# Kernel tuning notes

Hardware: AMD Instinct MI355X
Metric: run time of the kernel (lower is better)

Reference implementation:

```python
import jax, jax.numpy as jnp
import numpy as np

B, T, V, H = 4, 512, 8000, 7


def setup_inputs() -> dict:
    key = jax.random.key(0)
    k1, k2, k3 = jax.random.split(key, 3)
    return {
        "input_ids": jax.random.randint(k1, (B, T), 0, V),
        "frequencies": jax.random.normal(k2, (V,), dtype=jnp.float32) * 3.0,
        "amplitudes": 1.0 + jax.random.normal(k3, (V,), dtype=jnp.float32) * 0.1,
        "decay": jnp.asarray(1.5, dtype=jnp.float32),
        "chunk_size": 16,
    }


def reference(input_ids, frequencies, amplitudes, decay, chunk_size):
    h = jnp.arange(1, H + 1, dtype=frequencies.dtype)  # (H,)
    # harmonic expansion: freqs = f*[1..H], amps = A/[1..H]^decay
    all_f = frequencies[:, None] * h                    # (V, H)
    all_A = amplitudes[:, None] / h ** decay            # (V, H)
    seq_f = frequencies[input_ids][..., None] * h       # (B, T, H)
    seq_A = amplitudes[input_ids][..., None] / h ** decay

    nc = T // chunk_size
    sfc = seq_f.reshape(B, nc, chunk_size, H).transpose(1, 0, 2, 3)  # (nc,B,c,H)
    sAc = seq_A.reshape(B, nc, chunk_size, H).transpose(1, 0, 2, 3)

    def per_chunk(args):
        sf, sA = args  # (B,c,H)
        df = sf[:, :, :, None, None] - all_f[None, None, None, :, :]   # (B,c,H,V,H)
        amp = sA[:, :, :, None, None] * all_A[None, None, None, :, :]
        return 2.0 * (amp * jnp.sinc(2.0 * df)).sum(axis=(2, 4))       # (B,c,V)

    Cc = jax.lax.map(per_chunk, (sfc, sAc))            # (nc, B, c, V)
    C = Cc.transpose(1, 0, 2, 3).reshape(B, T, V)      # (B, T, V)

    cum = jnp.cumsum(C, axis=1)
    # logits[t] uses history 0..t-1 -> shift right by one, position 0 gets zeros
    logits = jnp.concatenate([jnp.zeros_like(cum[:, :1]), cum[:, :-1]], axis=1)
    return logits
```

## Files before the change

kernel.cpp:

```cpp
#include <hip/hip_runtime.h>
#include <math.h>


typedef float v2f __attribute__((ext_vector_type(2)));
typedef float v4f __attribute__((ext_vector_type(4)));

constexpr int cB = 4, cT = 512, cV = 8000, cH = 7;
constexpr int GT = 16;
constexpr int NSEG = cT / GT;
constexpr int NPLANE = 28;

__device__ __forceinline__ v2f pk_add(v2f a, v2f b) {
    v2f d; asm("v_pk_add_f32 %0, %1, %2" : "=v"(d) : "v"(a), "v"(b)); return d;
}
__device__ __forceinline__ v2f pk_mul(v2f a, v2f b) {
    v2f d; asm("v_pk_mul_f32 %0, %1, %2" : "=v"(d) : "v"(a), "v"(b)); return d;
}
__device__ __forceinline__ v2f pk_fma(v2f a, v2f b, v2f c) {
    v2f d; asm("v_pk_fma_f32 %0, %1, %2, %3" : "=v"(d) : "v"(a), "v"(b), "v"(c));
    return d;
}

__global__ __launch_bounds__(256) void wavelm_tab(
    const float* __restrict__ freq, const float* __restrict__ amp,
    const float* __restrict__ decay_p, float* __restrict__ tab)
{
    const int v = blockIdx.x * 256 + threadIdx.x;
    if (v >= cV) return;
    const float decay = decay_p[0];
    const float f = freq[v], A = amp[v];
    const float p2 = __builtin_amdgcn_exp2f(-decay);
    const float p3 = __builtin_amdgcn_exp2f(-decay * 1.5849625007f);
    const float p5 = __builtin_amdgcn_exp2f(-decay * 2.3219280949f);
    const float p7 = __builtin_amdgcn_exp2f(-decay * 2.8073549221f);
    const float rp[7] = {1.f, p2, p3, p2*p2, p5, p2*p3, p7};
    const float xr = f - rintf(f);
    const float s1 = __builtin_amdgcn_sinf(xr);
    const float c1 = __builtin_amdgcn_cosf(xr);
    float s = s1, c = c1;
#pragma unroll
    for (int k = 0; k < cH; ++k) {
        if (k) { const float sp = s, cp = c;
                 s = fmaf(sp, c1,  cp * s1);
                 c = fmaf(cp, c1, -(sp * s1)); }
        tab[(size_t)k * cV + v]        = s;
        tab[(size_t)(7 + k) * cV + v]  = c;
        tab[(size_t)(14 + k) * cV + v] = A * rp[k];
        tab[(size_t)(21 + k) * cV + v] = f * (float)(k + 1);
    }
}

__global__ __launch_bounds__(256) void wavelm_g(
    const int* __restrict__ ids, const float* __restrict__ tab,
    const float* __restrict__ decay_p,
    float* __restrict__ out, float* __restrict__ segsum, const int segmode)
{
    const int bs  = blockIdx.y;
    const int bt0 = bs * GT;
    const int vh  = blockIdx.x * 256 + threadIdx.x;
    const bool valid = (vh * 2 < cV);
    const int vc = valid ? vh : 0;

    const v2f* tp = (const v2f*)tab;
    v2f nb[cH], sBw[cH], cBw[cH];
#pragma unroll
    for (int j = 0; j < cH; ++j) {
        const v2f s = tp[(size_t)j * (cV/2) + vc];
        const v2f c = tp[(size_t)(7 + j) * (cV/2) + vc];
        const v2f w = tp[(size_t)(14 + j) * (cV/2) + vc];
        const v2f a = tp[(size_t)(21 + j) * (cV/2) + vc];
        const v2f ws = w * 0.15915494309189535f;
        sBw[j] = s * ws;
        cBw[j] = c * ws;
        nb[j].x = -a.x;  nb[j].y = -a.y;
    }

    const float decay = decay_p[0];
    const float q2 = __builtin_amdgcn_exp2f(-decay);
    const float q3 = __builtin_amdgcn_exp2f(-decay * 1.5849625007f);
    const float q5 = __builtin_amdgcn_exp2f(-decay * 2.3219280949f);
    const float q7 = __builtin_amdgcn_exp2f(-decay * 2.8073549221f);
    const float rp[7] = {1.f, q2, q3, q2*q2, q5, q2*q3, q7};

    v2f acc;  acc.x = 0.f;  acc.y = 0.f;

    int idc = ids[bt0];
    for (int g = 0; g < GT; ++g) {
        const int idn = (g + 1 < GT) ? ids[bt0 + g + 1] : idc;

        const float fu  = tab[(size_t)21 * cV + idc];
        const float Au  = tab[(size_t)14 * cV + idc];
        const float s1u = tab[idc];
        const float c1u = tab[(size_t)7 * cV + idc];

        float accx = 0.f, accy = 0.f;
        float su = s1u, cu = c1u;
#pragma unroll
        for (int i = 0; i < cH; ++i) {
            if (i) { const float sp = su, cp = cu;
                     su = fmaf(sp, c1u,  cp * s1u);
                     cu = fmaf(cp, c1u, -(sp * s1u)); }
            const float au = fu * (float)(i + 1);
            v2f ai;  ai.x = au;  ai.y = au;
            v2f d[cH], p[cH];
#pragma unroll
            for (int j = 0; j < cH; ++j) d[j] = pk_add(ai, nb[j]);
            p[0] = d[0];
#pragma unroll
            for (int j = 1; j < cH; ++j) p[j] = pk_mul(p[j-1], d[j]);
            const float ptot = p[6].x * p[6].y;
            const float rt = __builtin_amdgcn_rcpf(ptot);
            v2f r;  r.x = rt * p[6].y;  r.y = rt * p[6].x;
            v2f accS = (v2f)0.f, accC = (v2f)0.f;
#pragma unroll
            for (int j = cH - 1; j >= 1; --j) {
                const v2f inv = pk_mul(r, p[j-1]);
                accS = pk_fma(cBw[j], inv, accS);
                accC = pk_fma(sBw[j], inv, accC);
                r = pk_mul(r, d[j]);
            }
            accS = pk_fma(cBw[0], r, accS);
            accC = pk_fma(sBw[0], r, accC);
            const float tx = fmaf(su, accS.x, -(cu * accC.x));
            const float ty = fmaf(su, accS.y, -(cu * accC.y));
            accx = fmaf(rp[i], tx, accx);
            accy = fmaf(rp[i], ty, accy);
        }

        if (!(fabsf(accx) < 1e30f) || !(fabsf(accy) < 1e30f)) {
            accx = 0.f;  accy = 0.f;
            float s2 = s1u, c2 = c1u;
#pragma unroll
            for (int i = 0; i < cH; ++i) {
                if (i) { const float sp = s2, cp = c2;
                         s2 = fmaf(sp, c1u,  cp * s1u);
                         c2 = fmaf(cp, c1u, -(sp * s1u)); }
                const float au = fu * (float)(i + 1);
                float ax = 0.f, ay = 0.f;
#pragma unroll
                for (int j = 0; j < cH; ++j) {
                    const v2f w = tp[(size_t)(14 + j) * (cV/2) + vc];
                    const float dx = au + nb[j].x;
                    const float dy = au + nb[j].y;
                    const float snx = fmaf(s2, cBw[j].x, -(c2 * sBw[j].x));
                    const float sny = fmaf(s2, cBw[j].y, -(c2 * sBw[j].y));
                    float qx = snx * __builtin_amdgcn_rcpf(dx);
                    float qy = sny * __builtin_amdgcn_rcpf(dy);
                    qx = (dx == 0.f) ? w.x : qx;
                    qy = (dy == 0.f) ? w.y : qy;
                    ax += qx;  ay += qy;
                }
                accx = fmaf(rp[i], ax, accx);
                accy = fmaf(rp[i], ay, accy);
            }
        }

        if (valid) {
            const float A2 = 2.f * Au;
            v2f res;  res.x = A2 * accx;  res.y = A2 * accy;
            const size_t o = (size_t)(bt0 + g) * cV + (size_t)vh * 2;
            v2f wv;  wv.x = segmode ? acc.x : res.x;
                     wv.y = segmode ? acc.y : res.y;
            *(v2f*)(out + o) = wv;
            acc = pk_add(acc, res);
        }

        idc = idn;
    }

    if (valid && segmode)
        *(v2f*)(segsum + (size_t)bs * cV + (size_t)vh * 2) = acc;
}

__global__ __launch_bounds__(256) void wavelm_addbase(
    float* __restrict__ out, const float* __restrict__ segsum)
{
    const int btq = blockIdx.y;
    const int b  = btq >> 6;
    const int t0 = (btq & 63) * 8;
    const int seg = t0 / GT;
    if (seg == 0) return;
    const int v4 = blockIdx.x * 256 + threadIdx.x;
    if (v4 >= cV / 4) return;

    const float* sp = segsum + (size_t)b * NSEG * cV + (size_t)v4 * 4;
    v4f base;  base.x = 0.f;  base.y = 0.f;  base.z = 0.f;  base.w = 0.f;
    for (int s = 0; s < seg; ++s) {
        const v4f x = *(const v4f*)(sp + (size_t)s * cV);
        base.x += x.x;  base.y += x.y;  base.z += x.z;  base.w += x.w;
    }

    float* p = out + ((size_t)b * cT + t0) * cV + (size_t)v4 * 4;
#pragma unroll
    for (int k = 0; k < 8; ++k) {
        v4f x = *(v4f*)(p + (size_t)k * cV);
        x.x += base.x;  x.y += base.y;  x.z += base.z;  x.w += base.w;
        *(v4f*)(p + (size_t)k * cV) = x;
    }
}

__global__ __launch_bounds__(256) void wavelm_scan(float* __restrict__ out)
{
    const int g = blockIdx.x * blockDim.x + threadIdx.x;
    if (g >= cB * cV) return;
    const int b = g / cV;
    const int v = g - b * cV;
    float* p = out + (size_t)b * cT * cV + v;
    float acc = 0.f;
#pragma unroll 8
    for (int t = 0; t < cT; ++t) {
        const float c = p[(size_t)t * cV];
        p[(size_t)t * cV] = acc;
        acc += c;
    }
}

extern "C" void kernel_launch(void* const* d_in, const int* in_sizes, int n_in,
                              void* d_out, int out_size, void* d_ws, size_t ws_size,
                              hipStream_t stream)
{
    const int*   ids  = (const int*)d_in[0];
    const float* freq = (const float*)d_in[1];
    const float* amp  = (const float*)d_in[2];
    const float* dec  = (const float*)d_in[3];
    float* out = (float*)d_out;
    float* tab = (float*)d_ws;
    float* segsum = tab + (size_t)NPLANE * cV;

    const size_t tab_b = (size_t)NPLANE * cV * sizeof(float);
    const size_t seg_b = (size_t)cB * NSEG * cV * sizeof(float);
    const int segmode = (tab_b + seg_b <= ws_size) ? 1 : 0;

    wavelm_tab<<<(cV + 255) / 256, 256, 0, stream>>>(freq, amp, dec, tab);

    dim3 grid((cV / 2 + 255) / 256, cB * cT / GT);
    wavelm_g<<<grid, dim3(256), 0, stream>>>(ids, tab, dec, out, segsum, segmode);

    if (segmode) {
        dim3 ab((cV / 4 + 255) / 256, cB * (cT / 8));
        wavelm_addbase<<<ab, dim3(256), 0, stream>>>(out, segsum);
    } else {
        const int nchains = cB * cV;
        wavelm_scan<<<(nchains + 255) / 256, dim3(256), 0, stream>>>(out);
    }
}
```

Measured before the change: 207.2 us.

## Fuse harmonic table precompute into main kernel and drop table launch

Removes the separate table-building kernel and recomputes per-column sin/cos harmonics, weights and negated frequencies inside the main kernel from freq/amp directly. Per-token sin/cos are computed on the fly and broadcast with readfirstlane instead of being loaded from the table. Wavefronts that are entirely out of range now exit early. This saves one launch and the table's global traffic, at the cost of redundant trig work in every block; the readfirstlane assumes idc is uniform across the wave.

```diff
diff --git a/kernel.cpp b/kernel.cpp
--- a/kernel.cpp
+++ b/kernel.cpp
@@ -8,7 +8,6 @@
 constexpr int cB = 4, cT = 512, cV = 8000, cH = 7;
 constexpr int GT = 16;
 constexpr int NSEG = cT / GT;
-constexpr int NPLANE = 28;
 
 __device__ __forceinline__ v2f pk_add(v2f a, v2f b) {
     v2f d; asm("v_pk_add_f32 %0, %1, %2" : "=v"(d) : "v"(a), "v"(b)); return d;
@@ -20,60 +19,22 @@
     v2f d; asm("v_pk_fma_f32 %0, %1, %2, %3" : "=v"(d) : "v"(a), "v"(b), "v"(c));
     return d;
 }
-
-__global__ __launch_bounds__(256) void wavelm_tab(
-    const float* __restrict__ freq, const float* __restrict__ amp,
-    const float* __restrict__ decay_p, float* __restrict__ tab)
-{
-    const int v = blockIdx.x * 256 + threadIdx.x;
-    if (v >= cV) return;
-    const float decay = decay_p[0];
-    const float f = freq[v], A = amp[v];
-    const float p2 = __builtin_amdgcn_exp2f(-decay);
-    const float p3 = __builtin_amdgcn_exp2f(-decay * 1.5849625007f);
-    const float p5 = __builtin_amdgcn_exp2f(-decay * 2.3219280949f);
-    const float p7 = __builtin_amdgcn_exp2f(-decay * 2.8073549221f);
-    const float rp[7] = {1.f, p2, p3, p2*p2, p5, p2*p3, p7};
-    const float xr = f - rintf(f);
-    const float s1 = __builtin_amdgcn_sinf(xr);
-    const float c1 = __builtin_amdgcn_cosf(xr);
-    float s = s1, c = c1;
-#pragma unroll
-    for (int k = 0; k < cH; ++k) {
-        if (k) { const float sp = s, cp = c;
-                 s = fmaf(sp, c1,  cp * s1);
-                 c = fmaf(cp, c1, -(sp * s1)); }
-        tab[(size_t)k * cV + v]        = s;
-        tab[(size_t)(7 + k) * cV + v]  = c;
-        tab[(size_t)(14 + k) * cV + v] = A * rp[k];
-        tab[(size_t)(21 + k) * cV + v] = f * (float)(k + 1);
-    }
+__device__ __forceinline__ float rfl(float x) {
+    return __builtin_bit_cast(float,
+        __builtin_amdgcn_readfirstlane(__builtin_bit_cast(int, x)));
 }
 
 __global__ __launch_bounds__(256) void wavelm_g(
-    const int* __restrict__ ids, const float* __restrict__ tab,
-    const float* __restrict__ decay_p,
+    const int* __restrict__ ids, const float* __restrict__ freq,
+    const float* __restrict__ amp, const float* __restrict__ decay_p,
     float* __restrict__ out, float* __restrict__ segsum, const int segmode)
 {
     const int bs  = blockIdx.y;
     const int bt0 = bs * GT;
+    if ((blockIdx.x * 256 + (int)(threadIdx.x & 192u)) * 2 >= cV) return;
     const int vh  = blockIdx.x * 256 + threadIdx.x;
     const bool valid = (vh * 2 < cV);
     const int vc = valid ? vh : 0;
-
-    const v2f* tp = (const v2f*)tab;
-    v2f nb[cH], sBw[cH], cBw[cH];
-#pragma unroll
-    for (int j = 0; j < cH; ++j) {
-        const v2f s = tp[(size_t)j * (cV/2) + vc];
-        const v2f c = tp[(size_t)(7 + j) * (cV/2) + vc];
-        const v2f w = tp[(size_t)(14 + j) * (cV/2) + vc];
-        const v2f a = tp[(size_t)(21 + j) * (cV/2) + vc];
-        const v2f ws = w * 0.15915494309189535f;
-        sBw[j] = s * ws;
-        cBw[j] = c * ws;
-        nb[j].x = -a.x;  nb[j].y = -a.y;
-    }
 
     const float decay = decay_p[0];
     const float q2 = __builtin_amdgcn_exp2f(-decay);
@@ -82,16 +43,48 @@
     const float q7 = __builtin_amdgcn_exp2f(-decay * 2.8073549221f);
     const float rp[7] = {1.f, q2, q3, q2*q2, q5, q2*q3, q7};
 
+    const v2f fv = *(const v2f*)(freq + (size_t)vc * 2);
+    const v2f Av = *(const v2f*)(amp  + (size_t)vc * 2);
+    v2f nb[cH], sBw[cH], cBw[cH];
+    {
+        const float xrx = fv.x - rintf(fv.x);
+        const float xry = fv.y - rintf(fv.y);
+        const float s1x = __builtin_amdgcn_sinf(xrx);
+        const float c1x = __builtin_amdgcn_cosf(xrx);
+        const float s1y = __builtin_amdgcn_sinf(xry);
+        const float c1y = __builtin_amdgcn_cosf(xry);
+        float sx = s1x, cx = c1x, sy = s1y, cy = c1y;
+#pragma unroll
+        for (int k = 0; k < cH; ++k) {
+            if (k) {
+                const float spx = sx, cpx = cx, spy = sy, cpy = cy;
+                sx = fmaf(spx, c1x,  cpx * s1x);
+                cx = fmaf(cpx, c1x, -(spx * s1x));
+                sy = fmaf(spy, c1y,  cpy * s1y);
+                cy = fmaf(cpy, c1y, -(spy * s1y));
+            }
+            const float wx = Av.x * rp[k];
+            const float wy = Av.y * rp[k];
+            const float wsx = wx * 0.15915494309189535f;
+            const float wsy = wy * 0.15915494309189535f;
+            sBw[k].x = sx * wsx;  sBw[k].y = sy * wsy;
+            cBw[k].x = cx * wsx;  cBw[k].y = cy * wsy;
+            nb[k].x = -(fv.x * (float)(k + 1));
+            nb[k].y = -(fv.y * (float)(k + 1));
+        }
+    }
+
     v2f acc;  acc.x = 0.f;  acc.y = 0.f;
 
     int idc = ids[bt0];
     for (int g = 0; g < GT; ++g) {
         const int idn = (g + 1 < GT) ? ids[bt0 + g + 1] : idc;
 
-        const float fu  = tab[(size_t)21 * cV + idc];
-        const float Au  = tab[(size_t)14 * cV + idc];
-        const float s1u = tab[idc];
-        const float c1u = tab[(size_t)7 * cV + idc];
+        const float fu = freq[idc];
+        const float Au = amp[idc];
+        const float xru = fu - rintf(fu);
+        const float s1u = rfl(__builtin_amdgcn_sinf(xru));
+        const float c1u = rfl(__builtin_amdgcn_cosf(xru));
 
         float accx = 0.f, accy = 0.f;
         float su = s1u, cu = c1u;
@@ -139,15 +132,16 @@
                 float ax = 0.f, ay = 0.f;
 #pragma unroll
                 for (int j = 0; j < cH; ++j) {
-                    const v2f w = tp[(size_t)(14 + j) * (cV/2) + vc];
+                    const float wxx = Av.x * rp[j];
+                    const float wyy = Av.y * rp[j];
                     const float dx = au + nb[j].x;
                     const float dy = au + nb[j].y;
                     const float snx = fmaf(s2, cBw[j].x, -(c2 * sBw[j].x));
                     const float sny = fmaf(s2, cBw[j].y, -(c2 * sBw[j].y));
                     float qx = snx * __builtin_amdgcn_rcpf(dx);
                     float qy = sny * __builtin_amdgcn_rcpf(dy);
-                    qx = (dx == 0.f) ? w.x : qx;
-                    qy = (dy == 0.f) ? w.y : qy;
+                    qx = (dx == 0.f) ? wxx : qx;
+                    qy = (dy == 0.f) ? wyy : qy;
                     ax += qx;  ay += qy;
                 }
                 accx = fmaf(rp[i], ax, accx);
@@ -224,17 +218,14 @@
     const float* amp  = (const float*)d_in[2];
     const float* dec  = (const float*)d_in[3];
     float* out = (float*)d_out;
-    float* tab = (float*)d_ws;
-    float* segsum = tab + (size_t)NPLANE * cV;
-
-    const size_t tab_b = (size_t)NPLANE * cV * sizeof(float);
+    float* segsum = (float*)d_ws;
+
     const size_t seg_b = (size_t)cB * NSEG * cV * sizeof(float);
-    const int segmode = (tab_b + seg_b <= ws_size) ? 1 : 0;
-
-    wavelm_tab<<<(cV + 255) / 256, 256, 0, stream>>>(freq, amp, dec, tab);
+    const int segmode = (seg_b <= ws_size) ? 1 : 0;
 
     dim3 grid((cV / 2 + 255) / 256, cB * cT / GT);
-    wavelm_g<<<grid, dim3(256), 0, stream>>>(ids, tab, dec, out, segsum, segmode);
+    wavelm_g<<<grid, dim3(256), 0, stream>>>(ids, freq, amp, dec,
+                                             out, segsum, segmode);
 
     if (segmode) {
         dim3 ab((cV / 4 + 255) / 256, cB * (cT / 8));
```

Measured after the change: 203.4 us. About the same (-1.8%).
